# Performance work log

Hardware: AMD Instinct MI355X
Metric: run time of the kernel (lower is better)

Reference implementation:

```python
import jax, jax.numpy as jnp
import numpy as np

N_NODES = 50000
N_EDGES = 250000
D_IN, D_HID, D_OUT = 768, 256, 2


def _sage_conv(x, src, dst, W_l, b_l, W_r, n_nodes):
    # PyG SAGEConv (aggr='mean', root_weight=True):
    #   out[i] = lin_l(mean_{j in N(i)} x[j]) + lin_r(x[i])
    msg = x[src]  # [E, d] gather of source-node features
    agg = jax.ops.segment_sum(msg, dst, num_segments=n_nodes)
    cnt = jax.ops.segment_sum(jnp.ones((src.shape[0],), x.dtype), dst,
                              num_segments=n_nodes)
    agg = agg / jnp.maximum(cnt, 1.0)[:, None]
    return agg @ W_l.T + b_l + x @ W_r.T


def setup_inputs() -> dict:
    key = jax.random.key(0)
    ks = jax.random.split(key, 7)
    x = jax.random.normal(ks[0], (N_NODES, D_IN), dtype=jnp.float32)
    edge_index = jax.random.randint(ks[1], (2, N_EDGES), 0, N_NODES,
                                    dtype=jnp.int64)
    s1 = 1.0 / np.sqrt(D_IN)
    s2 = 1.0 / np.sqrt(D_HID)
    W1_l = jax.random.uniform(ks[2], (D_HID, D_IN), jnp.float32, -s1, s1)
    W1_r = jax.random.uniform(ks[3], (D_HID, D_IN), jnp.float32, -s1, s1)
    b1 = jnp.zeros((D_HID,), jnp.float32)
    W2_l = jax.random.uniform(ks[4], (D_OUT, D_HID), jnp.float32, -s2, s2)
    W2_r = jax.random.uniform(ks[5], (D_OUT, D_HID), jnp.float32, -s2, s2)
    b2 = jnp.zeros((D_OUT,), jnp.float32)
    return {"x": x, "edge_index": edge_index,
            "W1_l": W1_l, "b1": b1, "W1_r": W1_r,
            "W2_l": W2_l, "b2": b2, "W2_r": W2_r}


def reference(x, edge_index, W1_l, b1, W1_r, W2_l, b2, W2_r):
    src, dst = edge_index[0], edge_index[1]
    n = x.shape[0]
    h = _sage_conv(x, src, dst, W1_l, b1, W1_r, n)
    h = jax.nn.relu(h)
    # dropout is identity in eval mode (deterministic reference)
    out = _sage_conv(h, src, dst, W2_l, b2, W2_r, n)
    return out
```

## Files before the change

### kernel.cpp

```cpp
#include <hip/hip_runtime.h>
#include <stdint.h>


#define D_IN  768
#define D_HID 256
#define N1    512
#define KITERS (D_IN / 32)

typedef __attribute__((ext_vector_type(8))) short short8;
typedef __attribute__((ext_vector_type(4))) float f32x4;

__device__ __forceinline__ void async_copy16(const void* g, void* l) {
  __builtin_amdgcn_global_load_lds(
      (const __attribute__((address_space(1))) unsigned int*)g,
      (__attribute__((address_space(3))) unsigned int*)l,
      16, 0, 0);
}

__device__ __forceinline__ unsigned short f2bf(float f) {
  union { float f; unsigned u; } v; v.f = f;
  unsigned r = v.u + 0x7FFFu + ((v.u >> 16) & 1u);
  return (unsigned short)(r >> 16);
}

__device__ __forceinline__ float bf2f(unsigned short b) {
  union { unsigned u; float f; } v; v.u = ((unsigned)b) << 16;
  return v.f;
}

__global__ void prep_k(const void* __restrict__ eidx,
                       int* __restrict__ src32, int* __restrict__ dst32,
                       int* __restrict__ counts, int E,
                       const float* __restrict__ W1l, const float* __restrict__ W1r,
                       unsigned short* __restrict__ wb,
                       const float* __restrict__ x,
                       unsigned short* __restrict__ xb, int M, int Mp,
                       int gE, int gW) {
  const int tid = threadIdx.x;
  const int bid = blockIdx.x;

  if (bid < gE) {
    __shared__ int flag32;
    int i = bid * 256 + tid;
    unsigned v = (i < E) ? ((const unsigned int*)eidx)[2 * (size_t)i + 1] : 0u;
    unsigned long long any = __ballot(v != 0u);
    if (tid == 0) flag32 = 0;
    __syncthreads();
    if ((tid & 63) == 0 && any) flag32 = 1;
    __syncthreads();
    if (i >= E) return;
    int s, d;
    if (flag32) {
      const int* p = (const int*)eidx;
      s = p[i]; d = p[E + i];
    } else {
      const long long* p = (const long long*)eidx;
      s = (int)p[i]; d = (int)p[E + i];
    }
    src32[i] = s;
    dst32[i] = d;
    atomicAdd(&counts[d], 1);
    return;
  }

  if (bid < gE + gW) {
    int idx = (bid - gE) * 256 + tid;
    int total = N1 * (D_IN / 8);
    if (idx >= total) return;
    int row = idx / (D_IN / 8);
    int cpos = (idx % (D_IN / 8)) * 8;
    const float* p = (row < D_HID) ? (W1l + (size_t)row * D_IN + cpos)
                                   : (W1r + (size_t)(row - D_HID) * D_IN + cpos);
    float4 f0 = *(const float4*)p;
    float4 f1 = *(const float4*)(p + 4);
    short8 o;
    o[0] = (short)f2bf(f0.x); o[1] = (short)f2bf(f0.y);
    o[2] = (short)f2bf(f0.z); o[3] = (short)f2bf(f0.w);
    o[4] = (short)f2bf(f1.x); o[5] = (short)f2bf(f1.y);
    o[6] = (short)f2bf(f1.z); o[7] = (short)f2bf(f1.w);
    *(short8*)(wb + (size_t)idx * 8) = o;
    return;
  }

  {
    int idx = (bid - gE - gW) * 256 + tid;
    int total = Mp * (D_IN / 8);
    if (idx >= total) return;
    int row = idx / (D_IN / 8);
    short8 o;
    if (row < M) {
      int col = (idx % (D_IN / 8)) * 8;
      const float* p = x + (size_t)row * D_IN + col;
      float4 f0 = *(const float4*)p;
      float4 f1 = *(const float4*)(p + 4);
      o[0] = (short)f2bf(f0.x); o[1] = (short)f2bf(f0.y);
      o[2] = (short)f2bf(f0.z); o[3] = (short)f2bf(f0.w);
      o[4] = (short)f2bf(f1.x); o[5] = (short)f2bf(f1.y);
      o[6] = (short)f2bf(f1.z); o[7] = (short)f2bf(f1.w);
    } else {
      o = (short8)0;
    }
    *(short8*)(xb + (size_t)idx * 8) = o;
  }
}

__global__ void scanA_k(const int* __restrict__ counts,
                        int* __restrict__ blockSums, int M) {
  __shared__ int ts[256];
  int b = blockIdx.x, t = threadIdx.x;
  int base = b * 1024 + t * 4;
  int s = 0;
#pragma unroll
  for (int k = 0; k < 4; k++) { int i = base + k; if (i < M) s += counts[i]; }
  ts[t] = s;
  __syncthreads();
  for (int off = 128; off > 0; off >>= 1) {
    if (t < off) ts[t] += ts[t + off];
    __syncthreads();
  }
  if (t == 0) blockSums[b] = ts[0];
}

__global__ void scanC_k(const int* __restrict__ counts,
                        const int* __restrict__ bsums,
                        int* __restrict__ offs, int* __restrict__ cursor,
                        int M, int E, int nb) {
  __shared__ int ts[256];
  __shared__ int bofs;
  int b = blockIdx.x, t = threadIdx.x;
  if (t < 64) {
    int v = (t < nb) ? bsums[t] : 0;
    int orig = v;
#pragma unroll
    for (int off = 1; off < 64; off <<= 1) {
      int u = __shfl_up(v, off);
      if (t >= off) v += u;
    }
    if (t == b) bofs = v - orig;
  }
  int base = b * 1024 + t * 4;
  int v[4]; int s = 0;
#pragma unroll
  for (int k = 0; k < 4; k++) {
    int i = base + k;
    v[k] = (i < M) ? counts[i] : 0;
    s += v[k];
  }
  ts[t] = s;
  __syncthreads();
  for (int off = 1; off < 256; off <<= 1) {
    int x = (t >= off) ? ts[t - off] : 0;
    __syncthreads();
    ts[t] += x;
    __syncthreads();
  }
  int run = bofs + ts[t] - s;
#pragma unroll
  for (int k = 0; k < 4; k++) {
    int i = base + k;
    if (i < M) { offs[i] = run; cursor[i] = run; run += v[k]; }
  }
  if (b == 0 && t == 0) offs[M] = E;
}

__global__ void fill_k(const int* __restrict__ src, const int* __restrict__ dst,
                       int* __restrict__ cursor, int* __restrict__ csr, int E) {
  int i = blockIdx.x * 256 + threadIdx.x;
  if (i >= E) return;
  int pos = atomicAdd(&cursor[dst[i]], 1);
  csr[pos] = src[i];
}

__global__ __launch_bounds__(256) void gemm_k(
    const unsigned short* __restrict__ xb,
    const unsigned short* __restrict__ wb,
    unsigned short* __restrict__ Cl, unsigned short* __restrict__ Cr,
    int MT, int mtPerXcd) {
  __shared__ unsigned short As[2][128 * 32];
  __shared__ unsigned short Bs[2][128 * 32];

  const int bid = blockIdx.x;
  const int xcd = bid & 7;
  const int j   = bid >> 3;
  const int mt  = xcd * mtPerXcd + (j >> 2);
  if (mt >= MT) return;
  const int m0 = mt * 128;
  const int n0 = (j & 3) * 128;

  const int tid  = threadIdx.x;
  const int lane = tid & 63;
  const int wid  = tid >> 6;
  const int wr = wid >> 1, wc = wid & 1;
  const int l15  = lane & 15;
  const int quad = lane >> 4;

  const int arow0 = tid >> 2, akg = tid & 3;
  const unsigned short* axp0 = xb + (size_t)(m0 + arow0) * D_IN + akg * 8;
  const unsigned short* axp1 = xb + (size_t)(m0 + arow0 + 64) * D_IN + akg * 8;
  const int aoff0 = tid * 8;
  const int aoff1 = (tid + 256) * 8;

  const int brow = (tid >> 6) * 16 + (tid & 15);
  const int bcg  = (tid >> 4) & 3;
  const unsigned short* bgp0 = wb + (size_t)(n0 + brow) * D_IN + bcg * 8;
  const unsigned short* bgp1 = wb + (size_t)(n0 + brow + 64) * D_IN + bcg * 8;
  const int boff0 = tid * 8;
  const int boff1 = (tid + 256) * 8;

  f32x4 acc[4][4];
#pragma unroll
  for (int r = 0; r < 4; r++)
#pragma unroll
    for (int c = 0; c < 4; c++) acc[r][c] = (f32x4)0.0f;

#define STAGE(P, kk)                                                          \
  {                                                                           \
    const int kn = (kk) * 32;                                                 \
    async_copy16(axp0 + kn, &As[P][aoff0]);                                   \
    async_copy16(axp1 + kn, &As[P][aoff1]);                                   \
    async_copy16(bgp0 + kn, &Bs[P][boff0]);                                   \
    async_copy16(bgp1 + kn, &Bs[P][boff1]);                                   \
  }

#define READ_FRAGS(P, a, b)                                                   \
  _Pragma("unroll")                                                           \
  for (int r = 0; r < 4; r++)                                                 \
    a[r] = *(const short8*)&As[P][(wr * 64 + r * 16 + l15) * 32 + quad * 8];  \
  _Pragma("unroll")                                                           \
  for (int c = 0; c < 4; c++)                                                 \
    b[c] = *(const short8*)&Bs[P][(wc * 4 + c) * 512 + quad * 128 + l15 * 8];

#define MFMA16(a, b)                                                          \
  _Pragma("unroll")                                                           \
  for (int r = 0; r < 4; r++)                                                 \
    _Pragma("unroll")                                                         \
    for (int c = 0; c < 4; c++)                                               \
      acc[r][c] = __builtin_amdgcn_mfma_f32_16x16x32_bf16(a[r], b[c],         \
                                                          acc[r][c], 0, 0, 0);

#define GEMM_BODY(P, kk)                                                      \
  {                                                                           \
    short8 a[4], b[4];                                                        \
    READ_FRAGS(P, a, b)                                                       \
    asm volatile("s_waitcnt lgkmcnt(0)" ::: "memory");                        \
    __builtin_amdgcn_s_barrier();                                             \
    STAGE(P, (kk) + 2)                                                        \
    MFMA16(a, b)                                                              \
    asm volatile("s_waitcnt vmcnt(4)" ::: "memory");                          \
    __builtin_amdgcn_s_barrier();                                             \
  }

  STAGE(0, 0)
  STAGE(1, 1)
  asm volatile("s_waitcnt vmcnt(4)" ::: "memory");
  __builtin_amdgcn_s_barrier();

  for (int it = 0; it < KITERS - 2; it += 2) {
    GEMM_BODY(0, it)
    GEMM_BODY(1, it + 1)
  }

  {
    short8 a[4], b[4];
    READ_FRAGS(0, a, b)
    MFMA16(a, b)
    asm volatile("s_waitcnt vmcnt(0)" ::: "memory");
    __builtin_amdgcn_s_barrier();
  }
  {
    short8 a[4], b[4];
    READ_FRAGS(1, a, b)
    MFMA16(a, b)
  }
#undef GEMM_BODY
#undef MFMA16
#undef READ_FRAGS
#undef STAGE

  unsigned short* dstC = (n0 < 256) ? Cl : Cr;
  const int ncb = n0 & 255;
  const int crow0 = m0 + wr * 64;
  const int ccol0 = ncb + wc * 64;
#pragma unroll
  for (int r = 0; r < 4; r++)
#pragma unroll
    for (int c = 0; c < 4; c++) {
      int col = ccol0 + c * 16 + l15;
#pragma unroll
      for (int reg = 0; reg < 4; reg++) {
        int row = crow0 + r * 16 + quad * 4 + reg;
        dstC[(size_t)row * D_HID + col] = f2bf(acc[r][c][reg]);
      }
    }
}

__global__ void agg_l2_k(const unsigned short* __restrict__ Cl,
                         const unsigned short* __restrict__ Cr,
                         const int* __restrict__ offs, const int* __restrict__ csr,
                         const float* __restrict__ b1,
                         const float* __restrict__ W2l, const float* __restrict__ W2r,
                         float4* __restrict__ rs, int M) {
  int tid = threadIdx.x;
  int lane = tid & 63;
  int wid = tid >> 6;
  int i = blockIdx.x * 4 + wid;
  if (i >= M) return;
  int c = lane * 4;
  float4 bv  = *(const float4*)(b1 + c);
  float4 wl0 = *(const float4*)(W2l + c);
  float4 wl1 = *(const float4*)(W2l + D_HID + c);
  float4 wr0 = *(const float4*)(W2r + c);
  float4 wr1 = *(const float4*)(W2r + D_HID + c);
  int s = offs[i], e = offs[i + 1];
  ushort4 q = *(const ushort4*)(Cr + (size_t)i * D_HID + c);
  float a0x = 0.f, a0y = 0.f, a0z = 0.f, a0w = 0.f;
  float a1x = 0.f, a1y = 0.f, a1z = 0.f, a1w = 0.f;
  float a2x = 0.f, a2y = 0.f, a2z = 0.f, a2w = 0.f;
  float a3x = 0.f, a3y = 0.f, a3z = 0.f, a3w = 0.f;
  for (int base = s; base < e; base += 64) {
    int rem = e - base;
    int m = rem < 64 ? rem : 64;
    int jj = csr[base + (lane < m ? lane : m - 1)];
    int t = 0;
    for (; t + 4 <= m; t += 4) {
      int j0 = __shfl(jj, t);
      int j1 = __shfl(jj, t + 1);
      int j2 = __shfl(jj, t + 2);
      int j3 = __shfl(jj, t + 3);
      ushort4 v0 = *(const ushort4*)(Cl + (size_t)j0 * D_HID + c);
      ushort4 v1 = *(const ushort4*)(Cl + (size_t)j1 * D_HID + c);
      ushort4 v2 = *(const ushort4*)(Cl + (size_t)j2 * D_HID + c);
      ushort4 v3 = *(const ushort4*)(Cl + (size_t)j3 * D_HID + c);
      a0x += bf2f(v0.x); a0y += bf2f(v0.y); a0z += bf2f(v0.z); a0w += bf2f(v0.w);
      a1x += bf2f(v1.x); a1y += bf2f(v1.y); a1z += bf2f(v1.z); a1w += bf2f(v1.w);
      a2x += bf2f(v2.x); a2y += bf2f(v2.y); a2z += bf2f(v2.z); a2w += bf2f(v2.w);
      a3x += bf2f(v3.x); a3y += bf2f(v3.y); a3z += bf2f(v3.z); a3w += bf2f(v3.w);
    }
    for (; t < m; t++) {
      int j0 = __shfl(jj, t);
      ushort4 v = *(const ushort4*)(Cl + (size_t)j0 * D_HID + c);
      a0x += bf2f(v.x); a0y += bf2f(v.y); a0z += bf2f(v.z); a0w += bf2f(v.w);
    }
  }
  float ax = (a0x + a1x) + (a2x + a3x);
  float ay = (a0y + a1y) + (a2y + a3y);
  float az = (a0z + a1z) + (a2z + a3z);
  float aw = (a0w + a1w) + (a2w + a3w);
  float inv = 1.0f / fmaxf((float)(e - s), 1.0f);
  float h0 = fmaxf(ax * inv + bv.x + bf2f(q.x), 0.0f);
  float h1 = fmaxf(ay * inv + bv.y + bf2f(q.y), 0.0f);
  float h2 = fmaxf(az * inv + bv.z + bf2f(q.z), 0.0f);
  float h3 = fmaxf(aw * inv + bv.w + bf2f(q.w), 0.0f);
  float r0 = h0 * wl0.x + h1 * wl0.y + h2 * wl0.z + h3 * wl0.w;
  float r1 = h0 * wl1.x + h1 * wl1.y + h2 * wl1.z + h3 * wl1.w;
  float s0 = h0 * wr0.x + h1 * wr0.y + h2 * wr0.z + h3 * wr0.w;
  float s1 = h0 * wr1.x + h1 * wr1.y + h2 * wr1.z + h3 * wr1.w;
#pragma unroll
  for (int off = 32; off > 0; off >>= 1) {
    r0 += __shfl_xor(r0, off);
    r1 += __shfl_xor(r1, off);
    s0 += __shfl_xor(s0, off);
    s1 += __shfl_xor(s1, off);
  }
  if (lane == 0) rs[i] = make_float4(r0, r1, s0, s1);
}

__global__ void final_k(const float4* __restrict__ rs, const int* __restrict__ offs,
                        const int* __restrict__ csr, const float* __restrict__ b2,
                        float* __restrict__ out, int M) {
  int i = blockIdx.x * 256 + threadIdx.x;
  if (i >= M) return;
  int s = offs[i], e = offs[i + 1];
  float a0 = 0.0f, a1 = 0.0f, b0 = 0.0f, b1 = 0.0f;
  int t = s;
  for (; t + 2 <= e; t += 2) {
    float4 v0 = rs[csr[t]];
    float4 v1 = rs[csr[t + 1]];
    a0 += v0.x; a1 += v0.y;
    b0 += v1.x; b1 += v1.y;
  }
  if (t < e) { float4 v = rs[csr[t]]; a0 += v.x; a1 += v.y; }
  a0 += b0; a1 += b1;
  float inv = 1.0f / fmaxf((float)(e - s), 1.0f);
  float4 me = rs[i];
  out[2 * i + 0] = a0 * inv + b2[0] + me.z;
  out[2 * i + 1] = a1 * inv + b2[1] + me.w;
}


extern "C" void kernel_launch(void* const* d_in, const int* in_sizes, int n_in,
                              void* d_out, int out_size, void* d_ws, size_t ws_size,
                              hipStream_t stream) {
  const float* x   = (const float*)d_in[0];
  const void*  eix = d_in[1];
  const float* W1l = (const float*)d_in[2];
  const float* b1  = (const float*)d_in[3];
  const float* W1r = (const float*)d_in[4];
  const float* W2l = (const float*)d_in[5];
  const float* b2  = (const float*)d_in[6];
  const float* W2r = (const float*)d_in[7];
  float* out = (float*)d_out;

  const int M  = in_sizes[0] / D_IN;
  const int E  = in_sizes[1] / 2;
  const int Mp = ((M + 127) / 128) * 128;
  const int nb = (M + 1023) / 1024;
  const int MT = Mp / 128;
  const int mtPerXcd = (MT + 7) / 8;
  const int gemmBlocks = 8 * mtPerXcd * 4;

  char* ws = (char*)d_ws;
  size_t off = 0;
  auto alloc = [&](size_t b) { size_t o = off; off += (b + 255) & ~(size_t)255; return o; };
  size_t oCounts = alloc((size_t)M * 4);
  size_t zeroBytes = (size_t)M * 4;
  size_t oOffs   = alloc((size_t)(M + 1) * 4);
  size_t oCursor = alloc((size_t)M * 4);
  size_t oCsr    = alloc((size_t)E * 4);
  size_t oSrc    = alloc((size_t)E * 4);
  size_t oDst    = alloc((size_t)E * 4);
  size_t oBSums  = alloc(64 * 4);
  size_t oWb     = alloc((size_t)N1 * D_IN * 2);
  size_t oCl     = alloc((size_t)Mp * D_HID * 2);
  size_t oCr     = alloc((size_t)Mp * D_HID * 2);
  size_t oRs     = alloc((size_t)M * 16);
  size_t oXb     = alloc((size_t)Mp * D_IN * 2);
  (void)ws_size; (void)n_in; (void)out_size;

  int* counts = (int*)(ws + oCounts);
  int* offs   = (int*)(ws + oOffs);
  int* cursor = (int*)(ws + oCursor);
  int* csr    = (int*)(ws + oCsr);
  int* src32  = (int*)(ws + oSrc);
  int* dst32  = (int*)(ws + oDst);
  int* bsums  = (int*)(ws + oBSums);
  unsigned short* wb = (unsigned short*)(ws + oWb);
  unsigned short* Cl = (unsigned short*)(ws + oCl);
  unsigned short* Cr = (unsigned short*)(ws + oCr);
  float4* rs = (float4*)(ws + oRs);
  unsigned short* xb = (unsigned short*)(ws + oXb);

  hipMemsetAsync(counts, 0, zeroBytes, stream);

  int gE = (E + 255) / 256;
  int gW = (N1 * (D_IN / 8) + 255) / 256;
  int gX = (Mp * (D_IN / 8) + 255) / 256;
  prep_k<<<gE + gW + gX, 256, 0, stream>>>(eix, src32, dst32, counts, E,
                                           W1l, W1r, wb, x, xb, M, Mp, gE, gW);
  scanA_k<<<nb, 256, 0, stream>>>(counts, bsums, M);
  scanC_k<<<nb, 256, 0, stream>>>(counts, bsums, offs, cursor, M, E, nb);
  fill_k<<<(E + 255) / 256, 256, 0, stream>>>(src32, dst32, cursor, csr, E);

  gemm_k<<<gemmBlocks, 256, 0, stream>>>(xb, wb, Cl, Cr, MT, mtPerXcd);

  agg_l2_k<<<(M + 3) / 4, 256, 0, stream>>>(Cl, Cr, offs, csr, b1, W2l, W2r,
                                            rs, M);
  final_k<<<(M + 255) / 256, 256, 0, stream>>>(rs, offs, csr, b2, out, M);
}
```

Measured before the change: 376.2 us.

## Fuse fp32-to-bf16 conversion of x into GEMM A-tile loading

Removes the separate pass that converted x to a padded bf16 buffer and instead loads fp32 x rows directly in the GEMM. The rows are held in registers two stages ahead, converted with packed bf16 conversion instructions and written into LDS. This drops one full write and re-read of the bf16 copy of x, at the cost of more VGPRs and a reworked software pipeline with manual vmcnt accounting. Each GEMM block now reads the fp32 tile of x, twice the bytes of the bf16 copy, and does so for each of its four N tiles.

```diff
diff --git a/kernel.cpp b/kernel.cpp
--- a/kernel.cpp
+++ b/kernel.cpp
@@ -28,14 +28,20 @@
   return v.f;
 }
 
+__device__ __forceinline__ short8 cvt8(float4 a, float4 b) {
+  union { unsigned u[4]; short8 s; } r;
+  asm("v_cvt_pk_bf16_f32 %0, %1, %2" : "=v"(r.u[0]) : "v"(a.x), "v"(a.y));
+  asm("v_cvt_pk_bf16_f32 %0, %1, %2" : "=v"(r.u[1]) : "v"(a.z), "v"(a.w));
+  asm("v_cvt_pk_bf16_f32 %0, %1, %2" : "=v"(r.u[2]) : "v"(b.x), "v"(b.y));
+  asm("v_cvt_pk_bf16_f32 %0, %1, %2" : "=v"(r.u[3]) : "v"(b.z), "v"(b.w));
+  return r.s;
+}
+
 __global__ void prep_k(const void* __restrict__ eidx,
                        int* __restrict__ src32, int* __restrict__ dst32,
                        int* __restrict__ counts, int E,
                        const float* __restrict__ W1l, const float* __restrict__ W1r,
-                       unsigned short* __restrict__ wb,
-                       const float* __restrict__ x,
-                       unsigned short* __restrict__ xb, int M, int Mp,
-                       int gE, int gW) {
+                       unsigned short* __restrict__ wb, int gE) {
   const int tid = threadIdx.x;
   const int bid = blockIdx.x;
 
@@ -63,7 +69,7 @@
     return;
   }
 
-  if (bid < gE + gW) {
+  {
     int idx = (bid - gE) * 256 + tid;
     int total = N1 * (D_IN / 8);
     if (idx >= total) return;
@@ -79,28 +85,6 @@
     o[4] = (short)f2bf(f1.x); o[5] = (short)f2bf(f1.y);
     o[6] = (short)f2bf(f1.z); o[7] = (short)f2bf(f1.w);
     *(short8*)(wb + (size_t)idx * 8) = o;
-    return;
-  }
-
-  {
-    int idx = (bid - gE - gW) * 256 + tid;
-    int total = Mp * (D_IN / 8);
-    if (idx >= total) return;
-    int row = idx / (D_IN / 8);
-    short8 o;
-    if (row < M) {
-      int col = (idx % (D_IN / 8)) * 8;
-      const float* p = x + (size_t)row * D_IN + col;
-      float4 f0 = *(const float4*)p;
-      float4 f1 = *(const float4*)(p + 4);
-      o[0] = (short)f2bf(f0.x); o[1] = (short)f2bf(f0.y);
-      o[2] = (short)f2bf(f0.z); o[3] = (short)f2bf(f0.w);
-      o[4] = (short)f2bf(f1.x); o[5] = (short)f2bf(f1.y);
-      o[6] = (short)f2bf(f1.z); o[7] = (short)f2bf(f1.w);
-    } else {
-      o = (short8)0;
-    }
-    *(short8*)(xb + (size_t)idx * 8) = o;
   }
 }
 
@@ -172,10 +156,10 @@
 }
 
 __global__ __launch_bounds__(256) void gemm_k(
-    const unsigned short* __restrict__ xb,
+    const float* __restrict__ x,
     const unsigned short* __restrict__ wb,
     unsigned short* __restrict__ Cl, unsigned short* __restrict__ Cr,
-    int MT, int mtPerXcd) {
+    int M, int MT, int mtPerXcd) {
   __shared__ unsigned short As[2][128 * 32];
   __shared__ unsigned short Bs[2][128 * 32];
 
@@ -195,8 +179,8 @@
   const int quad = lane >> 4;
 
   const int arow0 = tid >> 2, akg = tid & 3;
-  const unsigned short* axp0 = xb + (size_t)(m0 + arow0) * D_IN + akg * 8;
-  const unsigned short* axp1 = xb + (size_t)(m0 + arow0 + 64) * D_IN + akg * 8;
+  const float* agp0 = x + (size_t)min(m0 + arow0, M - 1) * D_IN + akg * 8;
+  const float* agp1 = x + (size_t)min(m0 + arow0 + 64, M - 1) * D_IN + akg * 8;
   const int aoff0 = tid * 8;
   const int aoff1 = (tid + 256) * 8;
 
@@ -213,13 +197,29 @@
 #pragma unroll
     for (int c = 0; c < 4; c++) acc[r][c] = (f32x4)0.0f;
 
-#define STAGE(P, kk)                                                          \
+  float4 a0_0, a0_1, a0_2, a0_3;
+  float4 a1_0, a1_1, a1_2, a1_3;
+
+#define STAGEB(P, kk)                                                         \
   {                                                                           \
     const int kn = (kk) * 32;                                                 \
-    async_copy16(axp0 + kn, &As[P][aoff0]);                                   \
-    async_copy16(axp1 + kn, &As[P][aoff1]);                                   \
     async_copy16(bgp0 + kn, &Bs[P][boff0]);                                   \
     async_copy16(bgp1 + kn, &Bs[P][boff1]);                                   \
+  }
+
+#define LOADA(S0, S1, S2, S3, kk)                                             \
+  {                                                                           \
+    const int kn = (kk) * 32;                                                 \
+    S0 = *(const float4*)(agp0 + kn);                                         \
+    S1 = *(const float4*)(agp0 + kn + 4);                                     \
+    S2 = *(const float4*)(agp1 + kn);                                         \
+    S3 = *(const float4*)(agp1 + kn + 4);                                     \
+  }
+
+#define WRITEA(P, S0, S1, S2, S3)                                             \
+  {                                                                           \
+    *(short8*)&As[P][aoff0] = cvt8(S0, S1);                                   \
+    *(short8*)&As[P][aoff1] = cvt8(S2, S3);                                   \
   }
 
 #define READ_FRAGS(P, a, b)                                                   \
@@ -238,44 +238,49 @@
       acc[r][c] = __builtin_amdgcn_mfma_f32_16x16x32_bf16(a[r], b[c],         \
                                                           acc[r][c], 0, 0, 0);
 
-#define GEMM_BODY(P, kk)                                                      \
+#define GEMM_BODY(P, kk, S0, S1, S2, S3, VM)                                  \
   {                                                                           \
     short8 a[4], b[4];                                                        \
     READ_FRAGS(P, a, b)                                                       \
     asm volatile("s_waitcnt lgkmcnt(0)" ::: "memory");                        \
     __builtin_amdgcn_s_barrier();                                             \
-    STAGE(P, (kk) + 2)                                                        \
+    if ((kk) + 2 < KITERS) { STAGEB(P, (kk) + 2) }                            \
+    asm volatile("" ::: "memory");                                            \
+    if ((kk) + 2 < KITERS) { WRITEA(P, S0, S1, S2, S3) }                      \
+    if ((kk) + 4 < KITERS) { LOADA(S0, S1, S2, S3, (kk) + 4) }                \
+    asm volatile("" ::: "memory");                                            \
     MFMA16(a, b)                                                              \
-    asm volatile("s_waitcnt vmcnt(4)" ::: "memory");                          \
+    asm volatile("s_waitcnt vmcnt(" #VM ")" ::: "memory");                    \
     __builtin_amdgcn_s_barrier();                                             \
   }
 
-  STAGE(0, 0)
-  STAGE(1, 1)
-  asm volatile("s_waitcnt vmcnt(4)" ::: "memory");
+  STAGEB(0, 0)
+  STAGEB(1, 1)
+  asm volatile("" ::: "memory");
+  LOADA(a0_0, a0_1, a0_2, a0_3, 0)
+  LOADA(a1_0, a1_1, a1_2, a1_3, 1)
+  asm volatile("" ::: "memory");
+  WRITEA(0, a0_0, a0_1, a0_2, a0_3)
+  WRITEA(1, a1_0, a1_1, a1_2, a1_3)
+  LOADA(a0_0, a0_1, a0_2, a0_3, 2)
+  LOADA(a1_0, a1_1, a1_2, a1_3, 3)
+  asm volatile("s_waitcnt lgkmcnt(0)" ::: "memory");
   __builtin_amdgcn_s_barrier();
 
-  for (int it = 0; it < KITERS - 2; it += 2) {
-    GEMM_BODY(0, it)
-    GEMM_BODY(1, it + 1)
-  }
-
-  {
-    short8 a[4], b[4];
-    READ_FRAGS(0, a, b)
-    MFMA16(a, b)
-    asm volatile("s_waitcnt vmcnt(0)" ::: "memory");
-    __builtin_amdgcn_s_barrier();
-  }
-  {
-    short8 a[4], b[4];
-    READ_FRAGS(1, a, b)
-    MFMA16(a, b)
-  }
+  for (int it = 0; it < KITERS - 4; it += 2) {
+    { const int kk = it;     GEMM_BODY(0, kk, a0_0, a0_1, a0_2, a0_3, 6) }
+    { const int kk = it + 1; GEMM_BODY(1, kk, a1_0, a1_1, a1_2, a1_3, 6) }
+  }
+  { const int kk = 20; GEMM_BODY(0, kk, a0_0, a0_1, a0_2, a0_3, 2) }
+  { const int kk = 21; GEMM_BODY(1, kk, a1_0, a1_1, a1_2, a1_3, 2) }
+  { const int kk = 22; GEMM_BODY(0, kk, a0_0, a0_1, a0_2, a0_3, 0) }
+  { const int kk = 23; GEMM_BODY(1, kk, a1_0, a1_1, a1_2, a1_3, 0) }
 #undef GEMM_BODY
 #undef MFMA16
 #undef READ_FRAGS
-#undef STAGE
+#undef WRITEA
+#undef LOADA
+#undef STAGEB
 
   unsigned short* dstC = (n0 < 256) ? Cl : Cr;
   const int ncb = n0 & 255;
@@ -424,7 +429,6 @@
   size_t oCl     = alloc((size_t)Mp * D_HID * 2);
   size_t oCr     = alloc((size_t)Mp * D_HID * 2);
   size_t oRs     = alloc((size_t)M * 16);
-  size_t oXb     = alloc((size_t)Mp * D_IN * 2);
   (void)ws_size; (void)n_in; (void)out_size;
 
   int* counts = (int*)(ws + oCounts);
@@ -438,20 +442,18 @@
   unsigned short* Cl = (unsigned short*)(ws + oCl);
   unsigned short* Cr = (unsigned short*)(ws + oCr);
   float4* rs = (float4*)(ws + oRs);
-  unsigned short* xb = (unsigned short*)(ws + oXb);
 
   hipMemsetAsync(counts, 0, zeroBytes, stream);
 
   int gE = (E + 255) / 256;
   int gW = (N1 * (D_IN / 8) + 255) / 256;
-  int gX = (Mp * (D_IN / 8) + 255) / 256;
-  prep_k<<<gE + gW + gX, 256, 0, stream>>>(eix, src32, dst32, counts, E,
-                                           W1l, W1r, wb, x, xb, M, Mp, gE, gW);
+  prep_k<<<gE + gW, 256, 0, stream>>>(eix, src32, dst32, counts, E,
+                                      W1l, W1r, wb, gE);
   scanA_k<<<nb, 256, 0, stream>>>(counts, bsums, M);
   scanC_k<<<nb, 256, 0, stream>>>(counts, bsums, offs, cursor, M, E, nb);
   fill_k<<<(E + 255) / 256, 256, 0, stream>>>(src32, dst32, cursor, csr, E);
 
-  gemm_k<<<gemmBlocks, 256, 0, stream>>>(xb, wb, Cl, Cr, MT, mtPerXcd);
+  gemm_k<<<gemmBlocks, 256, 0, stream>>>(x, wb, Cl, Cr, M, MT, mtPerXcd);
 
   agg_l2_k<<<(M + 3) / 4, 256, 0, stream>>>(Cl, Cr, offs, csr, b1, W2l, W2r,
                                             rs, M);
```

After: 380.4 us. Within noise of the previous version (+1.1%).

## Fuse x fp32-to-bf16 conversion into GEMM A-tile loads

Applied to the files above, without the earlier changes.

Removes the separate pass that converted x to a bf16 copy in prep_k. The GEMM now streams fp32 x tiles straight into LDS and converts them to bf16 with packed cvt instructions when reading fragments. This drops one full write and re-read of a 50000x768 bf16 buffer. In exchange each of the four N-tile blocks reads fp32 A, twice the bytes of bf16, uses double the LDS for A, and adds conversion work inside the main loop.

```diff
diff --git a/kernel.cpp b/kernel.cpp
--- a/kernel.cpp
+++ b/kernel.cpp
@@ -28,14 +28,20 @@
   return v.f;
 }
 
+__device__ __forceinline__ short8 cvt8(float4 a, float4 b) {
+  union { unsigned u[4]; short8 s; } r;
+  asm("v_cvt_pk_bf16_f32 %0, %1, %2" : "=v"(r.u[0]) : "v"(a.x), "v"(a.y));
+  asm("v_cvt_pk_bf16_f32 %0, %1, %2" : "=v"(r.u[1]) : "v"(a.z), "v"(a.w));
+  asm("v_cvt_pk_bf16_f32 %0, %1, %2" : "=v"(r.u[2]) : "v"(b.x), "v"(b.y));
+  asm("v_cvt_pk_bf16_f32 %0, %1, %2" : "=v"(r.u[3]) : "v"(b.z), "v"(b.w));
+  return r.s;
+}
+
 __global__ void prep_k(const void* __restrict__ eidx,
                        int* __restrict__ src32, int* __restrict__ dst32,
                        int* __restrict__ counts, int E,
                        const float* __restrict__ W1l, const float* __restrict__ W1r,
-                       unsigned short* __restrict__ wb,
-                       const float* __restrict__ x,
-                       unsigned short* __restrict__ xb, int M, int Mp,
-                       int gE, int gW) {
+                       unsigned short* __restrict__ wb, int gE) {
   const int tid = threadIdx.x;
   const int bid = blockIdx.x;
 
@@ -63,7 +69,7 @@
     return;
   }
 
-  if (bid < gE + gW) {
+  {
     int idx = (bid - gE) * 256 + tid;
     int total = N1 * (D_IN / 8);
     if (idx >= total) return;
@@ -79,28 +85,6 @@
     o[4] = (short)f2bf(f1.x); o[5] = (short)f2bf(f1.y);
     o[6] = (short)f2bf(f1.z); o[7] = (short)f2bf(f1.w);
     *(short8*)(wb + (size_t)idx * 8) = o;
-    return;
-  }
-
-  {
-    int idx = (bid - gE - gW) * 256 + tid;
-    int total = Mp * (D_IN / 8);
-    if (idx >= total) return;
-    int row = idx / (D_IN / 8);
-    short8 o;
-    if (row < M) {
-      int col = (idx % (D_IN / 8)) * 8;
-      const float* p = x + (size_t)row * D_IN + col;
-      float4 f0 = *(const float4*)p;
-      float4 f1 = *(const float4*)(p + 4);
-      o[0] = (short)f2bf(f0.x); o[1] = (short)f2bf(f0.y);
-      o[2] = (short)f2bf(f0.z); o[3] = (short)f2bf(f0.w);
-      o[4] = (short)f2bf(f1.x); o[5] = (short)f2bf(f1.y);
-      o[6] = (short)f2bf(f1.z); o[7] = (short)f2bf(f1.w);
-    } else {
-      o = (short8)0;
-    }
-    *(short8*)(xb + (size_t)idx * 8) = o;
   }
 }
 
@@ -172,11 +156,11 @@
 }
 
 __global__ __launch_bounds__(256) void gemm_k(
-    const unsigned short* __restrict__ xb,
+    const float* __restrict__ x,
     const unsigned short* __restrict__ wb,
     unsigned short* __restrict__ Cl, unsigned short* __restrict__ Cr,
-    int MT, int mtPerXcd) {
-  __shared__ unsigned short As[2][128 * 32];
+    int M, int MT, int mtPerXcd) {
+  __shared__ float          Asf[2][128 * 32];
   __shared__ unsigned short Bs[2][128 * 32];
 
   const int bid = blockIdx.x;
@@ -194,11 +178,16 @@
   const int l15  = lane & 15;
   const int quad = lane >> 4;
 
-  const int arow0 = tid >> 2, akg = tid & 3;
-  const unsigned short* axp0 = xb + (size_t)(m0 + arow0) * D_IN + akg * 8;
-  const unsigned short* axp1 = xb + (size_t)(m0 + arow0 + 64) * D_IN + akg * 8;
-  const int aoff0 = tid * 8;
-  const int aoff1 = (tid + 256) * 8;
+  const float* aptr[4];
+  int adst[4];
+#pragma unroll
+  for (int c = 0; c < 4; c++) {
+    int g = c * 256 + tid;
+    int r = ((g >> 7) << 4) | (g & 15);
+    int kg = (g >> 4) & 7;
+    aptr[c] = x + (size_t)min(m0 + r, M - 1) * D_IN + kg * 4;
+    adst[c] = g * 4;
+  }
 
   const int brow = (tid >> 6) * 16 + (tid & 15);
   const int bcg  = (tid >> 4) & 3;
@@ -216,19 +205,25 @@
 #define STAGE(P, kk)                                                          \
   {                                                                           \
     const int kn = (kk) * 32;                                                 \
-    async_copy16(axp0 + kn, &As[P][aoff0]);                                   \
-    async_copy16(axp1 + kn, &As[P][aoff1]);                                   \
+    async_copy16(aptr[0] + kn, &Asf[P][adst[0]]);                             \
+    async_copy16(aptr[1] + kn, &Asf[P][adst[1]]);                             \
+    async_copy16(aptr[2] + kn, &Asf[P][adst[2]]);                             \
+    async_copy16(aptr[3] + kn, &Asf[P][adst[3]]);                             \
     async_copy16(bgp0 + kn, &Bs[P][boff0]);                                   \
     async_copy16(bgp1 + kn, &Bs[P][boff1]);                                   \
   }
 
 #define READ_FRAGS(P, a, b)                                                   \
   _Pragma("unroll")                                                           \
-  for (int r = 0; r < 4; r++)                                                 \
-    a[r] = *(const short8*)&As[P][(wr * 64 + r * 16 + l15) * 32 + quad * 8];  \
+  for (int c = 0; c < 4; c++)                                                 \
+    b[c] = *(const short8*)&Bs[P][(wc * 4 + c) * 512 + quad * 128 + l15 * 8]; \
   _Pragma("unroll")                                                           \
-  for (int c = 0; c < 4; c++)                                                 \
-    b[c] = *(const short8*)&Bs[P][(wc * 4 + c) * 512 + quad * 128 + l15 * 8];
+  for (int r = 0; r < 4; r++) {                                               \
+    const int o0 = ((wr * 4 + r) * 128 + quad * 32 + l15) * 4;                \
+    float4 f0 = *(const float4*)&Asf[P][o0];                                  \
+    float4 f1 = *(const float4*)&Asf[P][o0 + 64];                             \
+    a[r] = cvt8(f0, f1);                                                      \
+  }
 
 #define MFMA16(a, b)                                                          \
   _Pragma("unroll")                                                           \
@@ -238,27 +233,28 @@
       acc[r][c] = __builtin_amdgcn_mfma_f32_16x16x32_bf16(a[r], b[c],         \
                                                           acc[r][c], 0, 0, 0);
 
-#define GEMM_BODY(P, kk)                                                      \
+#define GEMM_BODY(P, kk, VM)                                                  \
   {                                                                           \
     short8 a[4], b[4];                                                        \
     READ_FRAGS(P, a, b)                                                       \
     asm volatile("s_waitcnt lgkmcnt(0)" ::: "memory");                        \
     __builtin_amdgcn_s_barrier();                                             \
-    STAGE(P, (kk) + 2)                                                        \
+    if ((kk) + 2 < KITERS) { STAGE(P, (kk) + 2) }                             \
     MFMA16(a, b)                                                              \
-    asm volatile("s_waitcnt vmcnt(4)" ::: "memory");                          \
+    asm volatile("s_waitcnt vmcnt(" #VM ")" ::: "memory");                    \
     __builtin_amdgcn_s_barrier();                                             \
   }
 
   STAGE(0, 0)
   STAGE(1, 1)
-  asm volatile("s_waitcnt vmcnt(4)" ::: "memory");
+  asm volatile("s_waitcnt vmcnt(6)" ::: "memory");
   __builtin_amdgcn_s_barrier();
 
   for (int it = 0; it < KITERS - 2; it += 2) {
-    GEMM_BODY(0, it)
-    GEMM_BODY(1, it + 1)
-  }
+    GEMM_BODY(0, it, 6)
+    GEMM_BODY(1, it + 1, 6)
+  }
+#undef GEMM_BODY
 
   {
     short8 a[4], b[4];
@@ -272,7 +268,6 @@
     READ_FRAGS(1, a, b)
     MFMA16(a, b)
   }
-#undef GEMM_BODY
 #undef MFMA16
 #undef READ_FRAGS
 #undef STAGE
@@ -424,7 +419,6 @@
   size_t oCl     = alloc((size_t)Mp * D_HID * 2);
   size_t oCr     = alloc((size_t)Mp * D_HID * 2);
   size_t oRs     = alloc((size_t)M * 16);
-  size_t oXb     = alloc((size_t)Mp * D_IN * 2);
   (void)ws_size; (void)n_in; (void)out_size;
 
   int* counts = (int*)(ws + oCounts);
@@ -438,20 +432,18 @@
   unsigned short* Cl = (unsigned short*)(ws + oCl);
   unsigned short* Cr = (unsigned short*)(ws + oCr);
   float4* rs = (float4*)(ws + oRs);
-  unsigned short* xb = (unsigned short*)(ws + oXb);
 
   hipMemsetAsync(counts, 0, zeroBytes, stream);
 
   int gE = (E + 255) / 256;
   int gW = (N1 * (D_IN / 8) + 255) / 256;
-  int gX = (Mp * (D_IN / 8) + 255) / 256;
-  prep_k<<<gE + gW + gX, 256, 0, stream>>>(eix, src32, dst32, counts, E,
-                                           W1l, W1r, wb, x, xb, M, Mp, gE, gW);
+  prep_k<<<gE + gW, 256, 0, stream>>>(eix, src32, dst32, counts, E,
+                                      W1l, W1r, wb, gE);
   scanA_k<<<nb, 256, 0, stream>>>(counts, bsums, M);
   scanC_k<<<nb, 256, 0, stream>>>(counts, bsums, offs, cursor, M, E, nb);
   fill_k<<<(E + 255) / 256, 256, 0, stream>>>(src32, dst32, cursor, csr, E);
 
-  gemm_k<<<gemmBlocks, 256, 0, stream>>>(xb, wb, Cl, Cr, MT, mtPerXcd);
+  gemm_k<<<gemmBlocks, 256, 0, stream>>>(x, wb, Cl, Cr, M, MT, mtPerXcd);
 
   agg_l2_k<<<(M + 3) / 4, 256, 0, stream>>>(Cl, Cr, offs, csr, b1, W2l, W2r,
                                             rs, M);
```

Result: slower. 413.2 us (+9.8%).

## Widen GEMM K-tile to 64, use 8 waves, and XOR-swizzle LDS A tile

Applied to the files above, without the earlier changes.

The layer-1 GEMM kernel now runs 512 threads (8 waves) per 128x128 tile instead of 4 waves, and stages K in chunks of 64 rather than 32, which halves the number of barrier-separated iterations. The A tile in LDS gets an XOR swizzle to avoid bank conflicts on the wider rows. Each wave now holds a 64x32 accumulator, which frees registers for higher occupancy. In exchange, LDS use per block doubles, and the prefetch guard and wait counts become more delicate.

```diff
diff --git a/kernel.cpp b/kernel.cpp
--- a/kernel.cpp
+++ b/kernel.cpp
@@ -5,7 +5,7 @@
 #define D_IN  768
 #define D_HID 256
 #define N1    512
-#define KITERS (D_IN / 32)
+#define KBODY 12
 
 typedef __attribute__((ext_vector_type(8))) short short8;
 typedef __attribute__((ext_vector_type(4))) float f32x4;
@@ -171,13 +171,13 @@
   csr[pos] = src[i];
 }
 
-__global__ __launch_bounds__(256) void gemm_k(
+__global__ __launch_bounds__(512, 4) void gemm_k(
     const unsigned short* __restrict__ xb,
     const unsigned short* __restrict__ wb,
     unsigned short* __restrict__ Cl, unsigned short* __restrict__ Cr,
     int MT, int mtPerXcd) {
-  __shared__ unsigned short As[2][128 * 32];
-  __shared__ unsigned short Bs[2][128 * 32];
+  __shared__ unsigned short As[2][128 * 64];
+  __shared__ unsigned short Bs[2][128 * 64];
 
   const int bid = blockIdx.x;
   const int xcd = bid & 7;
@@ -190,32 +190,36 @@
   const int tid  = threadIdx.x;
   const int lane = tid & 63;
   const int wid  = tid >> 6;
-  const int wr = wid >> 1, wc = wid & 1;
+  const int wr = wid >> 2, wc = wid & 3;
   const int l15  = lane & 15;
   const int quad = lane >> 4;
 
-  const int arow0 = tid >> 2, akg = tid & 3;
-  const unsigned short* axp0 = xb + (size_t)(m0 + arow0) * D_IN + akg * 8;
-  const unsigned short* axp1 = xb + (size_t)(m0 + arow0 + 64) * D_IN + akg * 8;
+  const int ar0 = tid >> 3, ac0 = (tid & 7) ^ (ar0 & 7);
+  const int ar1 = (tid + 512) >> 3, ac1 = (tid & 7) ^ (ar1 & 7);
+  const unsigned short* axp0 = xb + (size_t)(m0 + ar0) * D_IN + ac0 * 8;
+  const unsigned short* axp1 = xb + (size_t)(m0 + ar1) * D_IN + ac1 * 8;
   const int aoff0 = tid * 8;
-  const int aoff1 = (tid + 256) * 8;
-
-  const int brow = (tid >> 6) * 16 + (tid & 15);
-  const int bcg  = (tid >> 4) & 3;
-  const unsigned short* bgp0 = wb + (size_t)(n0 + brow) * D_IN + bcg * 8;
-  const unsigned short* bgp1 = wb + (size_t)(n0 + brow + 64) * D_IN + bcg * 8;
+  const int aoff1 = (tid + 512) * 8;
+
+  const int h1 = tid + 512;
+  const int brow0 = ((tid >> 7) << 4) + (tid & 15);
+  const int bk0   = (((tid >> 6) & 1) << 5) + (((tid >> 4) & 3) << 3);
+  const int brow1 = ((h1 >> 7) << 4) + (h1 & 15);
+  const int bk1   = (((h1 >> 6) & 1) << 5) + (((h1 >> 4) & 3) << 3);
+  const unsigned short* bgp0 = wb + (size_t)(n0 + brow0) * D_IN + bk0;
+  const unsigned short* bgp1 = wb + (size_t)(n0 + brow1) * D_IN + bk1;
   const int boff0 = tid * 8;
-  const int boff1 = (tid + 256) * 8;
-
-  f32x4 acc[4][4];
+  const int boff1 = (tid + 512) * 8;
+
+  f32x4 acc[4][2];
 #pragma unroll
   for (int r = 0; r < 4; r++)
 #pragma unroll
-    for (int c = 0; c < 4; c++) acc[r][c] = (f32x4)0.0f;
+    for (int c = 0; c < 2; c++) acc[r][c] = (f32x4)0.0f;
 
 #define STAGE(P, kk)                                                          \
   {                                                                           \
-    const int kn = (kk) * 32;                                                 \
+    const int kn = (kk) * 64;                                                 \
     async_copy16(axp0 + kn, &As[P][aoff0]);                                   \
     async_copy16(axp1 + kn, &As[P][aoff1]);                                   \
     async_copy16(bgp0 + kn, &Bs[P][boff0]);                                   \
@@ -225,28 +229,36 @@
 #define READ_FRAGS(P, a, b)                                                   \
   _Pragma("unroll")                                                           \
   for (int r = 0; r < 4; r++)                                                 \
-    a[r] = *(const short8*)&As[P][(wr * 64 + r * 16 + l15) * 32 + quad * 8];  \
+    _Pragma("unroll")                                                         \
+    for (int s = 0; s < 2; s++)                                               \
+      a[r][s] = *(const short8*)&As[P][(wr * 64 + r * 16 + l15) * 64 +        \
+                                       ((s * 4 + quad) ^ (l15 & 7)) * 8];     \
   _Pragma("unroll")                                                           \
-  for (int c = 0; c < 4; c++)                                                 \
-    b[c] = *(const short8*)&Bs[P][(wc * 4 + c) * 512 + quad * 128 + l15 * 8];
+  for (int c = 0; c < 2; c++)                                                 \
+    _Pragma("unroll")                                                         \
+    for (int s = 0; s < 2; s++)                                               \
+      b[c][s] = *(const short8*)&Bs[P][(wc * 2 + c) * 1024 + s * 512 +        \
+                                       quad * 128 + l15 * 8];
 
 #define MFMA16(a, b)                                                          \
   _Pragma("unroll")                                                           \
-  for (int r = 0; r < 4; r++)                                                 \
+  for (int s = 0; s < 2; s++)                                                 \
     _Pragma("unroll")                                                         \
-    for (int c = 0; c < 4; c++)                                               \
-      acc[r][c] = __builtin_amdgcn_mfma_f32_16x16x32_bf16(a[r], b[c],         \
-                                                          acc[r][c], 0, 0, 0);
-
-#define GEMM_BODY(P, kk)                                                      \
+    for (int r = 0; r < 4; r++)                                               \
+      _Pragma("unroll")                                                       \
+      for (int c = 0; c < 2; c++)                                             \
+        acc[r][c] = __builtin_amdgcn_mfma_f32_16x16x32_bf16(a[r][s], b[c][s], \
+                                                            acc[r][c], 0, 0, 0);
+
+#define GEMM_BODY(P, kk, VM)                                                  \
   {                                                                           \
-    short8 a[4], b[4];                                                        \
+    short8 a[4][2], b[2][2];                                                  \
     READ_FRAGS(P, a, b)                                                       \
     asm volatile("s_waitcnt lgkmcnt(0)" ::: "memory");                        \
     __builtin_amdgcn_s_barrier();                                             \
-    STAGE(P, (kk) + 2)                                                        \
+    if ((kk) + 2 < KBODY) { STAGE(P, (kk) + 2) }                              \
     MFMA16(a, b)                                                              \
-    asm volatile("s_waitcnt vmcnt(4)" ::: "memory");                          \
+    asm volatile("s_waitcnt vmcnt(" #VM ")" ::: "memory");                    \
     __builtin_amdgcn_s_barrier();                                             \
   }
 
@@ -255,21 +267,22 @@
   asm volatile("s_waitcnt vmcnt(4)" ::: "memory");
   __builtin_amdgcn_s_barrier();
 
-  for (int it = 0; it < KITERS - 2; it += 2) {
-    GEMM_BODY(0, it)
-    GEMM_BODY(1, it + 1)
-  }
-
+  for (int it = 0; it < KBODY - 2; it += 2) {
+    GEMM_BODY(0, it, 4)
+    GEMM_BODY(1, it + 1, 4)
+  }
   {
-    short8 a[4], b[4];
+    short8 a[4][2], b[2][2];
     READ_FRAGS(0, a, b)
+    asm volatile("s_waitcnt lgkmcnt(0)" ::: "memory");
     MFMA16(a, b)
     asm volatile("s_waitcnt vmcnt(0)" ::: "memory");
     __builtin_amdgcn_s_barrier();
   }
   {
-    short8 a[4], b[4];
+    short8 a[4][2], b[2][2];
     READ_FRAGS(1, a, b)
+    asm volatile("s_waitcnt lgkmcnt(0)" ::: "memory");
     MFMA16(a, b)
   }
 #undef GEMM_BODY
@@ -280,11 +293,11 @@
   unsigned short* dstC = (n0 < 256) ? Cl : Cr;
   const int ncb = n0 & 255;
   const int crow0 = m0 + wr * 64;
-  const int ccol0 = ncb + wc * 64;
+  const int ccol0 = ncb + wc * 32;
 #pragma unroll
   for (int r = 0; r < 4; r++)
 #pragma unroll
-    for (int c = 0; c < 4; c++) {
+    for (int c = 0; c < 2; c++) {
       int col = ccol0 + c * 16 + l15;
 #pragma unroll
       for (int reg = 0; reg < 4; reg++) {
@@ -451,7 +464,7 @@
   scanC_k<<<nb, 256, 0, stream>>>(counts, bsums, offs, cursor, M, E, nb);
   fill_k<<<(E + 255) / 256, 256, 0, stream>>>(src32, dst32, cursor, csr, E);
 
-  gemm_k<<<gemmBlocks, 256, 0, stream>>>(xb, wb, Cl, Cr, MT, mtPerXcd);
+  gemm_k<<<gemmBlocks, 512, 0, stream>>>(xb, wb, Cl, Cr, MT, mtPerXcd);
 
   agg_l2_k<<<(M + 3) / 4, 256, 0, stream>>>(Cl, Cr, offs, csr, b1, W2l, W2r,
                                             rs, M);
```

Result: faster. 365.8 us (-2.8%).
